# Performance work log

Hardware: AMD Instinct MI355X
Metric: run time of the kernel (lower is better)

## Reference

```python
import jax, jax.numpy as jnp
import numpy as np
import math

B, V, D = 16, 4096, 512
K, H = 64, 8
DK = D // H
DE = 16
DFF = 4 * D
EPS_MASK = 1e-6
EPS_DEN = 1e-8


def setup_inputs() -> dict:
    key = jax.random.key(0)
    ks = jax.random.split(key, 16)
    s = 0.02
    return {
        "x": jax.random.normal(ks[0], (B, V, D), jnp.float32),
        "assign": jax.random.uniform(ks[1], (B, V, K), jnp.float32),
        "E": jax.random.normal(ks[2], (K, DE), jnp.float32),
        "cls0": jax.random.normal(ks[3], (1, K, D), jnp.float32) * s,
        "E2D_w": jax.random.normal(ks[4], (DE, D), jnp.float32) * s,
        "E2D_b": jnp.zeros((D,), jnp.float32),
        "Wq_w": jax.random.normal(ks[5], (D, D), jnp.float32) * s,
        "Wq_b": jnp.zeros((D,), jnp.float32),
        "Wk_w": jax.random.normal(ks[6], (D, D), jnp.float32) * s,
        "Wk_b": jnp.zeros((D,), jnp.float32),
        "Wv_w": jax.random.normal(ks[7], (D, D), jnp.float32) * s,
        "Wv_b": jnp.zeros((D,), jnp.float32),
        "ln_g": jnp.ones((D,), jnp.float32),
        "ln_b": jnp.zeros((D,), jnp.float32),
        "fc1_w": jax.random.normal(ks[8], (D, DFF), jnp.float32) * s,
        "fc1_b": jnp.zeros((DFF,), jnp.float32),
        "fc2_w": jax.random.normal(ks[9], (DFF, D), jnp.float32) * s,
        "fc2_b": jnp.zeros((D,), jnp.float32),
    }


def _layernorm(x, g, b):
    mu = x.mean(-1, keepdims=True)
    var = ((x - mu) ** 2).mean(-1, keepdims=True)
    return (x - mu) / jnp.sqrt(var + 1e-5) * g + b


def reference(x, assign, E, cls0, E2D_w, E2D_b, Wq_w, Wq_b, Wk_w, Wk_b, Wv_w, Wv_b,
              ln_g, ln_b, fc1_w, fc1_b, fc2_w, fc2_b):
    # CLS tokens modulated by module embeddings: [B,K,D]
    cls = jnp.broadcast_to(cls0, (B, K, D)) + (E @ E2D_w + E2D_b)[None]

    # detached mask (transpose of assign): [B,K,V]
    mask_kv = jax.lax.stop_gradient(jnp.swapaxes(assign, 1, 2))
    count_per_k = mask_kv.sum(-1)                 # [B,K]
    empty_mask = count_per_k <= 1e-6              # [B,K]

    # projections -> heads
    q = (_layernorm(cls, ln_g, ln_b) @ Wq_w + Wq_b).reshape(B, K, H, DK)
    k = (x @ Wk_w + Wk_b).reshape(B, V, H, DK)
    v = (x @ Wv_w + Wv_b).reshape(B, V, H, DK)

    # logits [B,H,K,V]
    logits = jnp.einsum("bkhd,bvhd->bhkv", q, k) / math.sqrt(DK)
    log_mask = jnp.log(jnp.clip(mask_kv, 0.0, 1.0) + EPS_MASK)[:, None]  # [B,1,K,V]
    scores = logits + log_mask
    scores = scores - scores.max(-1, keepdims=True)
    attn = jnp.exp(scores)
    attn = attn / (attn.sum(-1, keepdims=True) + EPS_DEN)

    # weighted values, merge heads -> [B,K,D]
    m = jnp.einsum("bhkv,bvhd->bkhd", attn, v).reshape(B, K, D)

    # empty-slot fallback
    m = jnp.where(empty_mask[..., None], cls, m)

    # FFN residual (LayerNorm shared with q path); eval mode: dropout off
    h = _layernorm(m, ln_g, ln_b)
    h = jax.nn.gelu(h @ fc1_w + fc1_b, approximate=False) @ fc2_w + fc2_b
    m = m + h
    return m, count_per_k, empty_mask
```

## Files before the change

kernel.cpp:

```cpp
#include <hip/hip_runtime.h>
#include <hip/hip_bf16.h>
#include <cstdint>
#include <cmath>

#define DEV static __device__ __forceinline__

typedef __attribute__((ext_vector_type(8))) short bf16x8;
typedef __attribute__((ext_vector_type(4))) float f32x4;

DEV ushort f2bf(float f) {
    union { float f; uint32_t u; } v; v.f = f;
    uint32_t r = v.u + 0x7FFFu + ((v.u >> 16) & 1u);
    return (ushort)(r >> 16);
}
DEV uint32_t pack2bf(float lo, float hi) {
    return (uint32_t)f2bf(lo) | ((uint32_t)f2bf(hi) << 16);
}
DEV float bf2f(ushort h) {
    union { uint32_t u; float f; } v; v.u = ((uint32_t)h) << 16;
    return v.f;
}
DEV void gld16(const ushort* g, ushort* l) {
    __builtin_amdgcn_global_load_lds(
        (const __attribute__((address_space(1))) unsigned int*)g,
        (__attribute__((address_space(3))) unsigned int*)l, 16, 0, 0);
}

__global__ __launch_bounds__(256)
void prep_all_k(int nxb, const float* __restrict__ x, ushort* __restrict__ xb,
                const float* __restrict__ E, const float* __restrict__ cls0,
                const float* __restrict__ e2dw, const float* __restrict__ e2db,
                const float* __restrict__ lng, const float* __restrict__ lnbv,
                const float* __restrict__ wq, const float* __restrict__ wqb,
                float* __restrict__ cls, ushort* __restrict__ qbf,
                const float* __restrict__ wk, const float* __restrict__ wv,
                const float* __restrict__ fc1w, const float* __restrict__ fc2w,
                const float* __restrict__ kb, const float* __restrict__ vb,
                ushort* __restrict__ wkvt, ushort* __restrict__ fc1t,
                ushort* __restrict__ fc2t, float* __restrict__ biaskv,
                const float* __restrict__ assign, float* __restrict__ cpart)
{
    __shared__ float sh[64 * 65];
    int id = blockIdx.x;
    const int tid = threadIdx.x;

    if (id < nxb) {
        const size_t i = (size_t)id * 256 + tid;
        const float4* s = (const float4*)(x + i * 8);
        float4 a = s[0], b = s[1];
        uint4 o;
        o.x = pack2bf(a.x, a.y); o.y = pack2bf(a.z, a.w);
        o.z = pack2bf(b.x, b.y); o.w = pack2bf(b.z, b.w);
        *(uint4*)(xb + i * 8) = o;
        return;
    }
    id -= nxb;
    if (id < 64) {
        const int k = id;
        float* lnv = sh;
        float* Ek = sh + 512;
        float2* red = (float2*)(sh + 544);
        if (tid < 16) Ek[tid] = E[k * 16 + tid];
        __syncthreads();
        float vals[2];
#pragma unroll
        for (int j = 0; j < 2; j++) {
            int d = tid + j * 256;
            float a = cls0[k * 512 + d] + e2db[d];
#pragma unroll
            for (int e = 0; e < 16; e++) a += Ek[e] * e2dw[e * 512 + d];
            vals[j] = a;
            cls[k * 512 + d] = a;
        }
        red[tid] = make_float2(vals[0] + vals[1],
                               vals[0] * vals[0] + vals[1] * vals[1]);
        __syncthreads();
        for (int s2 = 128; s2 > 0; s2 >>= 1) {
            if (tid < s2) {
                float2 o = red[tid + s2];
                float2 m = red[tid];
                red[tid] = make_float2(m.x + o.x, m.y + o.y);
            }
            __syncthreads();
        }
        float2 sr = red[0];
        float mu = sr.x * (1.f / 512.f);
        float var = sr.y * (1.f / 512.f) - mu * mu;
        float inv = rsqrtf(var + 1e-5f);
        __syncthreads();
#pragma unroll
        for (int j = 0; j < 2; j++) {
            int d = tid + j * 256;
            lnv[d] = (vals[j] - mu) * inv * lng[d] + lnbv[d];
        }
        __syncthreads();
#pragma unroll
        for (int j = 0; j < 2; j++) {
            int n = tid + j * 256;
            float acc = 0.f;
            for (int d = 0; d < 512; ++d)
                acc += lnv[d] * wq[d * 512 + n];
            qbf[k * 512 + n] = f2bf(acc + wqb[n]);
        }
        return;
    }
    id -= 64;
    if (id < 2564) {
        if (id >= 2560) {
            int i = (id - 2560) * 256 + tid;
            biaskv[i] = (i < 512) ? kb[i] : vb[i - 512];
            return;
        }
        const float* in; ushort* out; int R, C, bx, by;
        if (id < 256)        { in = wk;   out = wkvt;             R = 512;  C = 512;  int t = id;        bx = t & 15; by = t >> 4; }
        else if (id < 512)   { in = wv;   out = wkvt + 512 * 512; R = 512;  C = 512;  int t = id - 256;  bx = t & 15; by = t >> 4; }
        else if (id < 1536)  { in = fc1w; out = fc1t;             R = 512;  C = 2048; int t = id - 512;  bx = t & 63; by = t >> 6; }
        else                 { in = fc2w; out = fc2t;             R = 2048; C = 512;  int t = id - 1536; bx = t & 15; by = t >> 4; }
        float (*T)[33] = (float (*)[33])sh;
        const int c0 = bx * 32, r0 = by * 32;
        const int tx = tid & 31, ty = tid >> 5;
#pragma unroll
        for (int i = 0; i < 32; i += 8)
            T[ty + i][tx] = in[(size_t)(r0 + ty + i) * C + c0 + tx];
        __syncthreads();
#pragma unroll
        for (int i = 0; i < 32; i += 8)
            out[(size_t)(c0 + ty + i) * R + r0 + tx] = f2bf(T[tx][ty + i]);
        return;
    }
    id -= 2564;
    {
        const int vt = id & 63, b = id >> 6;
        float (*T)[65] = (float (*)[65])sh;
        const int rr = tid >> 2, sg = tid & 3;
        const float4* src = (const float4*)(assign + ((size_t)b * 4096 + vt * 64 + rr) * 64 + sg * 16);
        float4 a0 = src[0], a1 = src[1], a2 = src[2], a3 = src[3];
        float* tr = &T[rr][sg * 16];
        tr[0] = a0.x; tr[1] = a0.y; tr[2] = a0.z; tr[3] = a0.w;
        tr[4] = a1.x; tr[5] = a1.y; tr[6] = a1.z; tr[7] = a1.w;
        tr[8] = a2.x; tr[9] = a2.y; tr[10] = a2.z; tr[11] = a2.w;
        tr[12] = a3.x; tr[13] = a3.y; tr[14] = a3.z; tr[15] = a3.w;
        __syncthreads();
        const int k = rr;
        float ssum = 0.f;
#pragma unroll
        for (int j = 0; j < 4; j++)
#pragma unroll
            for (int t2 = 0; t2 < 4; t2++) ssum += T[sg * 16 + j * 4 + t2][k];
        ssum += __shfl_xor(ssum, 1, 64);
        ssum += __shfl_xor(ssum, 2, 64);
        if (sg == 0) cpart[((size_t)b * 64 + k) * 64 + vt] = ssum;
    }
}

template<int AMODE, int EPI, int SWZ, int ND, int KD, int LDK>
__global__ __launch_bounds__(512)
void gemm_k(const void* __restrict__ Ap, const ushort* __restrict__ Bt,
            const float* __restrict__ bias,
            ushort* __restrict__ o_bf, const float* __restrict__ res,
            float* __restrict__ o_f)
{
    __shared__ ushort smem[16384];
    ushort* As = smem;
    ushort* Bs = smem + 8192;
    int m0, n0;
    if (SWZ) {
        int L = blockIdx.x;
        int c = L & 7, j = L >> 3;
        m0 = (c * 64 + (j >> 3)) * 128;
        n0 = (j & 7) * 128;
    } else {
        m0 = blockIdx.x * 128;
        n0 = blockIdx.y * 128;
    }
    const int tid = threadIdx.x;
    const int w = tid >> 6, l = tid & 63;
    const int wr = w >> 2, wc = w & 3;
    const int lg = l >> 4, lr = l & 15;

    const f32x4 fzero = {0.f, 0.f, 0.f, 0.f};
    f32x4 acc[4][2];
#pragma unroll
    for (int i = 0; i < 4; i++)
#pragma unroll
        for (int j = 0; j < 2; j++) acc[i][j] = fzero;

    const int lrow8 = l >> 3;
    const int colswz = ((l & 7) ^ lrow8) * 8;
    const ushort* gB  = Bt + (size_t)(n0 + w * 16 + lrow8) * LDK + colswz;
    const ushort* gA0 = (const ushort*)Ap + (size_t)(m0 + w * 16 + lrow8) * LDK + colswz;
    const float*  gA1 = (const float*)Ap + (size_t)(m0 + w * 16 + (l >> 2)) * LDK + (l & 3) * 16;

    const int kbase = blockIdx.z * KD;
    constexpr int NT = KD / 64;
#pragma unroll
    for (int t = 0; t < NT; ++t) {
        const int kt = kbase + t * 64;
        __syncthreads();
        if (AMODE == 0) {
#pragma unroll
            for (int i = 0; i < 2; i++) {
                gld16(gA0 + (size_t)i * 8 * LDK + kt, As + (w * 16 + i * 8) * 64);
                gld16(gB + (size_t)i * 8 * LDK + kt, Bs + (w * 16 + i * 8) * 64);
            }
        } else {
            float4 av[4];
#pragma unroll
            for (int i = 0; i < 4; i++)
                av[i] = *(const float4*)(gA1 + kt + i * 4);
#pragma unroll
            for (int i = 0; i < 2; i++)
                gld16(gB + (size_t)i * 8 * LDK + kt, Bs + (w * 16 + i * 8) * 64);
            {
                int r = w * 16 + (l >> 2);
                uint2 p0, p1;
                p0.x = pack2bf(av[0].x, av[0].y); p0.y = pack2bf(av[0].z, av[0].w);
                uint2 q0; q0.x = pack2bf(av[1].x, av[1].y); q0.y = pack2bf(av[1].z, av[1].w);
                p1.x = pack2bf(av[2].x, av[2].y); p1.y = pack2bf(av[2].z, av[2].w);
                uint2 q1; q1.x = pack2bf(av[3].x, av[3].y); q1.y = pack2bf(av[3].z, av[3].w);
                int cb = (l & 3) * 32;
                *(uint2*)((char*)As + r * 128 + ((cb     ) ^ ((r & 7) << 4))) = p0;
                *(uint2*)((char*)As + r * 128 + ((cb +  8) ^ ((r & 7) << 4))) = q0;
                *(uint2*)((char*)As + r * 128 + ((cb + 16) ^ ((r & 7) << 4))) = p1;
                *(uint2*)((char*)As + r * 128 + ((cb + 24) ^ ((r & 7) << 4))) = q1;
            }
        }
        asm volatile("s_waitcnt vmcnt(0)" ::: "memory");
        __syncthreads();
#pragma unroll
        for (int kk = 0; kk < 2; kk++) {
            int kb = (kk * 32 + lg * 8) * 2;
            bf16x8 af[4], bfv[2];
#pragma unroll
            for (int mi = 0; mi < 4; mi++) {
                int row = wr * 64 + mi * 16 + lr;
                af[mi] = *(bf16x8*)((char*)As + row * 128 + (kb ^ ((row & 7) << 4)));
            }
#pragma unroll
            for (int ni = 0; ni < 2; ni++) {
                int row = wc * 32 + ni * 16 + lr;
                bfv[ni] = *(bf16x8*)((char*)Bs + row * 128 + (kb ^ ((row & 7) << 4)));
            }
#pragma unroll
            for (int mi = 0; mi < 4; mi++)
#pragma unroll
                for (int ni = 0; ni < 2; ni++)
                    acc[mi][ni] = __builtin_amdgcn_mfma_f32_16x16x32_bf16(af[mi], bfv[ni], acc[mi][ni], 0, 0, 0);
        }
    }

    if (EPI == 0) {
        __syncthreads();
#pragma unroll
        for (int mi = 0; mi < 4; mi++)
#pragma unroll
            for (int ni = 0; ni < 2; ni++)
#pragma unroll
                for (int r = 0; r < 4; r++) {
                    int rl = wr * 64 + mi * 16 + lg * 4 + r;
                    int cl = wc * 32 + ni * 16 + lr;
                    int byteoff = rl * 256 + ((cl * 2) ^ ((rl & 7) << 4));
                    *(ushort*)((char*)smem + byteoff) = f2bf(acc[mi][ni][r] + bias[n0 + cl]);
                }
        __syncthreads();
        const int row = tid >> 2, sg2 = tid & 3;
        uint4* dq = (uint4*)(o_bf + (size_t)(m0 + row) * ND + n0 + sg2 * 32);
#pragma unroll
        for (int q2 = 0; q2 < 4; q2++) {
            int byteoff = row * 256 + ((sg2 * 64 + q2 * 16) ^ ((row & 7) << 4));
            dq[q2] = *(const uint4*)((char*)smem + byteoff);
        }
    } else {
        float* ofz = o_f;
        if (EPI == 3)
            ofz = o_f + (size_t)blockIdx.z * (size_t)gridDim.x * 128 * ND;
#pragma unroll
        for (int mi = 0; mi < 4; mi++) {
#pragma unroll
            for (int ni = 0; ni < 2; ni++) {
#pragma unroll
                for (int r = 0; r < 4; r++) {
                    int row = m0 + wr * 64 + mi * 16 + lg * 4 + r;
                    int col = n0 + wc * 32 + ni * 16 + lr;
                    if (EPI == 1) {
                        float c = acc[mi][ni][r] + bias[col];
                        float gg = 0.5f * c * (1.f + erff(c * 0.70710678f));
                        o_bf[(size_t)row * ND + col] = f2bf(gg);
                    } else if (EPI == 2) {
                        float c = acc[mi][ni][r] + bias[col];
                        o_f[(size_t)row * ND + col] = c + res[(size_t)row * ND + col];
                    } else {
                        ofz[(size_t)row * ND + col] = acc[mi][ni][r];
                    }
                }
            }
        }
    }
}

__global__ __launch_bounds__(256)
void combine2_k(const float* __restrict__ fcp, const float* __restrict__ fc2b,
                float* __restrict__ mout)
{
    const int i = blockIdx.x * 256 + threadIdx.x;
    const int col = i & 511;
    float s = fc2b[col] + fcp[i] + fcp[i + 524288] + fcp[i + 2 * 524288] + fcp[i + 3 * 524288];
    mout[i] += s;
}

__global__ __launch_bounds__(256)
void attn_k(const ushort* __restrict__ qbf, const ushort* __restrict__ kv,
            const float* __restrict__ assign,
            float* __restrict__ partO, float* __restrict__ partML)
{
    const int h = blockIdx.x, s = blockIdx.y, b = blockIdx.z;
    __shared__ ushort Qs[64 * 64];
    __shared__ ushort Ks[64 * 64];
    __shared__ ushort Vt[64 * 64];
    __shared__ ushort Ps[64 * 64];
    __shared__ float  Lm[64 * 64];
    const int tid = threadIdx.x;
    const int w = tid >> 6, l = tid & 63, lg = l >> 4, lr = l & 15;
    const int rr = tid >> 2, qt = tid & 3;

    {
        const uint4* src = (const uint4*)(qbf + rr * 512 + h * 64 + qt * 16);
        uint4 t0 = src[0], t1 = src[1];
        int kb = qt * 32;
        *(uint4*)((char*)Qs + rr * 128 + ( kb       ^ ((rr & 7) << 4))) = t0;
        *(uint4*)((char*)Qs + rr * 128 + ((kb + 16) ^ ((rr & 7) << 4))) = t1;
    }

    const f32x4 fzero = {0.f, 0.f, 0.f, 0.f};
    f32x4 oacc[4];
#pragma unroll
    for (int ni = 0; ni < 4; ni++) oacc[ni] = fzero;
    float m_run[4], l_run[4];
#pragma unroll
    for (int r = 0; r < 4; r++) { m_run[r] = -3e38f; l_run[r] = 0.f; }

    const int v00 = s * 1024;

    for (int c = 0; c < 16; ++c) {
        const int vb = v00 + c * 64;
        __syncthreads();
        {
            const size_t rowb = ((size_t)b * 4096 + vb + rr) * 1024 + h * 64;
            const uint4* srck = (const uint4*)(kv + rowb + qt * 16);
            uint4 k0 = srck[0], k1 = srck[1];
            int kb = qt * 32;
            *(uint4*)((char*)Ks + rr * 128 + ( kb       ^ ((rr & 7) << 4))) = k0;
            *(uint4*)((char*)Ks + rr * 128 + ((kb + 16) ^ ((rr & 7) << 4))) = k1;
            const ushort* srcv = kv + rowb + 512 + qt * 16;
            ushort vvv[16];
            *(uint4*)&vvv[0] = ((const uint4*)srcv)[0];
            *(uint4*)&vvv[8] = ((const uint4*)srcv)[1];
#pragma unroll
            for (int i = 0; i < 16; i++) {
                int dk = qt * 16 + i;
                *(ushort*)((char*)Vt + dk * 128 + ((rr * 2) ^ ((dk & 7) << 4))) = vvv[i];
            }
            const float4* srca = (const float4*)(assign + ((size_t)b * 4096 + vb + rr) * 64 + qt * 16);
            float4 A0 = srca[0], A1 = srca[1], A2 = srca[2], A3 = srca[3];
            float av[16] = {A0.x, A0.y, A0.z, A0.w, A1.x, A1.y, A1.z, A1.w,
                            A2.x, A2.y, A2.z, A2.w, A3.x, A3.y, A3.z, A3.w};
#pragma unroll
            for (int i = 0; i < 16; i++)
                Lm[(qt * 16 + i) * 64 + rr] = __logf(fminf(fmaxf(av[i], 0.f), 1.f) + 1e-6f);
        }
        __syncthreads();

        f32x4 sacc[4];
#pragma unroll
        for (int ni = 0; ni < 4; ni++) sacc[ni] = fzero;
        __builtin_amdgcn_s_setprio(1);
#pragma unroll
        for (int kk = 0; kk < 2; kk++) {
            int kb = (kk * 32 + lg * 8) * 2;
            int qrow = w * 16 + lr;
            bf16x8 aq = *(bf16x8*)((char*)Qs + qrow * 128 + (kb ^ ((qrow & 7) << 4)));
#pragma unroll
            for (int ni = 0; ni < 4; ni++) {
                int kr = ni * 16 + lr;
                bf16x8 bk = *(bf16x8*)((char*)Ks + kr * 128 + (kb ^ ((kr & 7) << 4)));
                sacc[ni] = __builtin_amdgcn_mfma_f32_16x16x32_bf16(aq, bk, sacc[ni], 0, 0, 0);
            }
        }
        __builtin_amdgcn_s_setprio(0);
        float sv[4][4], mx[4];
#pragma unroll
        for (int r = 0; r < 4; r++) {
            int q = w * 16 + lg * 4 + r;
            float m_ = -3e38f;
#pragma unroll
            for (int ni = 0; ni < 4; ni++) {
                float xx = sacc[ni][r] * 0.125f + Lm[q * 64 + ni * 16 + lr];
                sv[ni][r] = xx;
                m_ = fmaxf(m_, xx);
            }
            mx[r] = m_;
        }
#pragma unroll
        for (int off = 1; off < 16; off <<= 1)
#pragma unroll
            for (int r = 0; r < 4; r++) mx[r] = fmaxf(mx[r], __shfl_xor(mx[r], off, 64));
        float scale[4], lad[4];
#pragma unroll
        for (int r = 0; r < 4; r++) {
            float mn = fmaxf(m_run[r], mx[r]);
            scale[r] = __expf(m_run[r] - mn);
            m_run[r] = mn;
            float ls = 0.f;
#pragma unroll
            for (int ni = 0; ni < 4; ni++) {
                float p = __expf(sv[ni][r] - mn);
                sv[ni][r] = p;
                ls += p;
            }
            lad[r] = ls;
        }
#pragma unroll
        for (int off = 1; off < 16; off <<= 1)
#pragma unroll
            for (int r = 0; r < 4; r++) lad[r] += __shfl_xor(lad[r], off, 64);
#pragma unroll
        for (int r = 0; r < 4; r++) l_run[r] = l_run[r] * scale[r] + lad[r];
#pragma unroll
        for (int ni = 0; ni < 4; ni++) {
            f32x4 o = oacc[ni];
            o[0] *= scale[0]; o[1] *= scale[1]; o[2] *= scale[2]; o[3] *= scale[3];
            oacc[ni] = o;
        }
#pragma unroll
        for (int ni = 0; ni < 4; ni++)
#pragma unroll
            for (int r = 0; r < 4; r++) {
                int q = w * 16 + lg * 4 + r;
                int key = ni * 16 + lr;
                *(ushort*)((char*)Ps + q * 128 + ((key * 2) ^ ((q & 7) << 4))) = f2bf(sv[ni][r]);
            }
        __builtin_amdgcn_s_setprio(1);
#pragma unroll
        for (int kk = 0; kk < 2; kk++) {
            int kb = (kk * 32 + lg * 8) * 2;
            int prow = w * 16 + lr;
            bf16x8 ap = *(bf16x8*)((char*)Ps + prow * 128 + (kb ^ ((prow & 7) << 4)));
#pragma unroll
            for (int ni = 0; ni < 4; ni++) {
                int dk = ni * 16 + lr;
                bf16x8 bv = *(bf16x8*)((char*)Vt + dk * 128 + (kb ^ ((dk & 7) << 4)));
                oacc[ni] = __builtin_amdgcn_mfma_f32_16x16x32_bf16(ap, bv, oacc[ni], 0, 0, 0);
            }
        }
        __builtin_amdgcn_s_setprio(0);
    }
    const size_t ob = ((size_t)((b * 8 + h) * 4 + s)) * 4096;
#pragma unroll
    for (int ni = 0; ni < 4; ni++)
#pragma unroll
        for (int r = 0; r < 4; r++) {
            int q = w * 16 + lg * 4 + r;
            int dk = ni * 16 + lr;
            partO[ob + q * 64 + dk] = oacc[ni][r];
        }
    if (lr == 0) {
#pragma unroll
        for (int r = 0; r < 4; r++) {
            int q = w * 16 + lg * 4 + r;
            partML[((b * 8 + h) * 4 + s) * 128 + q * 2 + 0] = m_run[r];
            partML[((b * 8 + h) * 4 + s) * 128 + q * 2 + 1] = l_run[r];
        }
    }
}

__global__ __launch_bounds__(256)
void combine_k(const float* __restrict__ partO, const float* __restrict__ partML,
               const float* __restrict__ cls, const float* __restrict__ cpart,
               float* __restrict__ cnt, float* __restrict__ emp,
               float* __restrict__ mout)
{
    const int bh = blockIdx.x, b = bh >> 3, h = bh & 7;
    __shared__ float Ms[64], Ls[64], Cs[64];
    const int tid = threadIdx.x;
    if (tid < 64) {
        float M = -3e38f;
#pragma unroll
        for (int s2 = 0; s2 < 4; s2++) M = fmaxf(M, partML[(bh * 4 + s2) * 128 + tid * 2]);
        float L = 0.f;
#pragma unroll
        for (int s2 = 0; s2 < 4; s2++) {
            float m_ = partML[(bh * 4 + s2) * 128 + tid * 2];
            float l_ = partML[(bh * 4 + s2) * 128 + tid * 2 + 1];
            L += l_ * __expf(m_ - M);
        }
        Ms[tid] = M; Ls[tid] = L;
        const float4* p = (const float4*)(cpart + ((size_t)b * 64 + tid) * 64);
        float cs = 0.f;
#pragma unroll
        for (int t = 0; t < 16; t++) {
            float4 f = p[t];
            cs += f.x + f.y + f.z + f.w;
        }
        Cs[tid] = cs;
        if (h == 0) {
            cnt[b * 64 + tid] = cs;
            emp[b * 64 + tid] = (cs <= 1e-6f) ? 1.f : 0.f;
        }
    }
    __syncthreads();
#pragma unroll
    for (int i = 0; i < 16; i++) {
        int e = i * 256 + tid;
        int q = e >> 6, dk = e & 63;
        float o = 0.f;
#pragma unroll
        for (int s2 = 0; s2 < 4; s2++) {
            float m_ = partML[(bh * 4 + s2) * 128 + q * 2];
            o += partO[(size_t)(bh * 4 + s2) * 4096 + e] * __expf(m_ - Ms[q]);
        }
        float val = o / (Ls[q] + 1e-8f);
        if (Cs[q] <= 1e-6f) val = cls[q * 512 + h * 64 + dk];
        mout[((size_t)b * 64 + q) * 512 + h * 64 + dk] = val;
    }
}

__global__ __launch_bounds__(256)
void ln_rows_k(const float* __restrict__ m, const float* __restrict__ g,
               const float* __restrict__ be, ushort* __restrict__ out)
{
    const int r = blockIdx.x, tid = threadIdx.x;
    float v0 = m[(size_t)r * 512 + tid];
    float v1 = m[(size_t)r * 512 + tid + 256];
    __shared__ float2 red[256];
    red[tid] = make_float2(v0 + v1, v0 * v0 + v1 * v1);
    __syncthreads();
    for (int s2 = 128; s2 > 0; s2 >>= 1) {
        if (tid < s2) {
            float2 o = red[tid + s2];
            float2 m2 = red[tid];
            red[tid] = make_float2(m2.x + o.x, m2.y + o.y);
        }
        __syncthreads();
    }
    float2 sr = red[0];
    float mu = sr.x * (1.f / 512.f);
    float var = sr.y * (1.f / 512.f) - mu * mu;
    float inv = rsqrtf(var + 1e-5f);
    out[(size_t)r * 512 + tid]       = f2bf((v0 - mu) * inv * g[tid] + be[tid]);
    out[(size_t)r * 512 + tid + 256] = f2bf((v1 - mu) * inv * g[tid + 256] + be[tid + 256]);
}

extern "C" void kernel_launch(void* const* d_in, const int* in_sizes, int n_in,
                              void* d_out, int out_size, void* d_ws, size_t ws_size,
                              hipStream_t stream)
{
    const float* x      = (const float*)d_in[0];
    const float* assign = (const float*)d_in[1];
    const float* E      = (const float*)d_in[2];
    const float* cls0   = (const float*)d_in[3];
    const float* e2dw   = (const float*)d_in[4];
    const float* e2db   = (const float*)d_in[5];
    const float* wq     = (const float*)d_in[6];
    const float* wqb    = (const float*)d_in[7];
    const float* wk     = (const float*)d_in[8];
    const float* wkb    = (const float*)d_in[9];
    const float* wv     = (const float*)d_in[10];
    const float* wvb    = (const float*)d_in[11];
    const float* lng    = (const float*)d_in[12];
    const float* lnbv   = (const float*)d_in[13];
    const float* fc1w   = (const float*)d_in[14];
    const float* fc1b   = (const float*)d_in[15];
    const float* fc2w   = (const float*)d_in[16];
    const float* fc2b   = (const float*)d_in[17];

    float* mout = (float*)d_out;
    float* cnt  = mout + (size_t)16 * 64 * 512;
    float* emp  = cnt + 16 * 64;

    char* ws = (char*)d_ws;
    size_t off = 0;
    auto alloc = [&](size_t bytes) -> char* {
        char* p = ws + off;
        off = (off + bytes + 255) & ~(size_t)255;
        return p;
    };
    float*  cls    = (float*) alloc((size_t)64 * 512 * 4);
    ushort* qbf    = (ushort*)alloc((size_t)64 * 512 * 2);
    ushort* wkvt   = (ushort*)alloc((size_t)1024 * 512 * 2);
    float*  biaskv = (float*) alloc((size_t)1024 * 4);
    ushort* fc1t   = (ushort*)alloc((size_t)2048 * 512 * 2);
    ushort* fc2t   = (ushort*)alloc((size_t)512 * 2048 * 2);
    ushort* kvb    = (ushort*)alloc((size_t)16 * 4096 * 1024 * 2);
    float*  partO  = (float*) alloc((size_t)16 * 8 * 4 * 64 * 64 * 4);
    float*  partML = (float*) alloc((size_t)16 * 8 * 4 * 128 * 4);
    float*  cpart  = (float*) alloc((size_t)16 * 64 * 64 * 4);
    ushort* lnbf   = (ushort*)alloc((size_t)1024 * 512 * 2);
    ushort* hhb    = (ushort*)alloc((size_t)1024 * 2048 * 2);
    float*  fcp    = (float*) alloc((size_t)4 * 1024 * 512 * 4);
    ushort* xb     = (ushort*)alloc((size_t)16 * 4096 * 512 * 2);
    const bool use_xb = (off <= ws_size);

    const int nxb = use_xb ? 16384 : 0;
    prep_all_k<<<nxb + 64 + 2564 + 1024, 256, 0, stream>>>(
        nxb, x, xb, E, cls0, e2dw, e2db, lng, lnbv, wq, wqb, cls, qbf,
        wk, wv, fc1w, fc2w, wkb, wvb, wkvt, fc1t, fc2t, biaskv,
        assign, cpart);

    if (use_xb) {
        gemm_k<0, 0, 1, 1024, 512, 512><<<4096, 512, 0, stream>>>(xb, wkvt, biaskv,
                                                                  kvb, nullptr, nullptr);
    } else {
        gemm_k<1, 0, 1, 1024, 512, 512><<<4096, 512, 0, stream>>>(x, wkvt, biaskv,
                                                                  kvb, nullptr, nullptr);
    }
    attn_k<<<dim3(8, 4, 16), 256, 0, stream>>>(qbf, kvb, assign, partO, partML);
    combine_k<<<128, 256, 0, stream>>>(partO, partML, cls, cpart, cnt, emp, mout);
    ln_rows_k<<<1024, 256, 0, stream>>>(mout, lng, lnbv, lnbf);
    gemm_k<0, 1, 0, 2048, 512, 512><<<dim3(8, 16), 512, 0, stream>>>(lnbf, fc1t, fc1b,
                                                                     hhb, nullptr, nullptr);
    gemm_k<0, 3, 0, 512, 512, 2048><<<dim3(8, 4, 4), 512, 0, stream>>>(hhb, fc2t, fc2b,
                                                                       nullptr, nullptr, fcp);
    combine2_k<<<2048, 256, 0, stream>>>(fcp, fc2b, mout);
}
```

Baseline: 275.0 us.

## Fuse fp32-to-bf16 x conversion into KV GEMM via direct-to-LDS fp32 loads

Removes the separate pass that converted x to a bf16 buffer in the prep kernel. The KV projection GEMM now loads fp32 x tiles straight into LDS with global_load_lds using an XOR swizzle, then converts to bf16 with packed cvt instructions when building MFMA fragments. This drops a full write and re-read of the 64 MB bf16 copy of x. In exchange the GEMM reads twice as many A bytes per tile, needs more LDS per block, and does conversion work that is repeated for each of the 8 N-tiles.

```diff
diff --git a/kernel.cpp b/kernel.cpp
--- a/kernel.cpp
+++ b/kernel.cpp
@@ -13,9 +13,6 @@
     uint32_t r = v.u + 0x7FFFu + ((v.u >> 16) & 1u);
     return (ushort)(r >> 16);
 }
-DEV uint32_t pack2bf(float lo, float hi) {
-    return (uint32_t)f2bf(lo) | ((uint32_t)f2bf(hi) << 16);
-}
 DEV float bf2f(ushort h) {
     union { uint32_t u; float f; } v; v.u = ((uint32_t)h) << 16;
     return v.f;
@@ -25,10 +22,19 @@
         (const __attribute__((address_space(1))) unsigned int*)g,
         (__attribute__((address_space(3))) unsigned int*)l, 16, 0, 0);
 }
+DEV bf16x8 cvt8(float4 a, float4 b) {
+    uint32_t u0, u1, u2, u3;
+    asm("v_cvt_pk_bf16_f32 %0, %1, %2" : "=v"(u0) : "v"(a.x), "v"(a.y));
+    asm("v_cvt_pk_bf16_f32 %0, %1, %2" : "=v"(u1) : "v"(a.z), "v"(a.w));
+    asm("v_cvt_pk_bf16_f32 %0, %1, %2" : "=v"(u2) : "v"(b.x), "v"(b.y));
+    asm("v_cvt_pk_bf16_f32 %0, %1, %2" : "=v"(u3) : "v"(b.z), "v"(b.w));
+    union { uint4 u; bf16x8 h; } r;
+    r.u = make_uint4(u0, u1, u2, u3);
+    return r.h;
+}
 
 __global__ __launch_bounds__(256)
-void prep_all_k(int nxb, const float* __restrict__ x, ushort* __restrict__ xb,
-                const float* __restrict__ E, const float* __restrict__ cls0,
+void prep_all_k(const float* __restrict__ E, const float* __restrict__ cls0,
                 const float* __restrict__ e2dw, const float* __restrict__ e2db,
                 const float* __restrict__ lng, const float* __restrict__ lnbv,
                 const float* __restrict__ wq, const float* __restrict__ wqb,
@@ -44,17 +50,6 @@
     int id = blockIdx.x;
     const int tid = threadIdx.x;
 
-    if (id < nxb) {
-        const size_t i = (size_t)id * 256 + tid;
-        const float4* s = (const float4*)(x + i * 8);
-        float4 a = s[0], b = s[1];
-        uint4 o;
-        o.x = pack2bf(a.x, a.y); o.y = pack2bf(a.z, a.w);
-        o.z = pack2bf(b.x, b.y); o.w = pack2bf(b.z, b.w);
-        *(uint4*)(xb + i * 8) = o;
-        return;
-    }
-    id -= nxb;
     if (id < 64) {
         const int k = id;
         float* lnv = sh;
@@ -160,9 +155,10 @@
             ushort* __restrict__ o_bf, const float* __restrict__ res,
             float* __restrict__ o_f)
 {
-    __shared__ ushort smem[16384];
-    ushort* As = smem;
-    ushort* Bs = smem + 8192;
+    __shared__ ushort smem[(AMODE == 2) ? 24576 : 16384];
+    float*  Asf = (float*)smem;
+    ushort* As  = smem;
+    ushort* Bs  = smem + ((AMODE == 2) ? 16384 : 8192);
     int m0, n0;
     if (SWZ) {
         int L = blockIdx.x;
@@ -189,7 +185,13 @@
     const int colswz = ((l & 7) ^ lrow8) * 8;
     const ushort* gB  = Bt + (size_t)(n0 + w * 16 + lrow8) * LDK + colswz;
     const ushort* gA0 = (const ushort*)Ap + (size_t)(m0 + w * 16 + lrow8) * LDK + colswz;
-    const float*  gA1 = (const float*)Ap + (size_t)(m0 + w * 16 + (l >> 2)) * LDK + (l & 3) * 16;
+    const float* gA2[4];
+#pragma unroll
+    for (int i = 0; i < 4; i++) {
+        int rloc = i * 4 + (l >> 4);
+        gA2[i] = (const float*)Ap + (size_t)(m0 + w * 16 + rloc) * LDK
+                 + (((l & 15) ^ rloc) << 2);
+    }
 
     const int kbase = blockIdx.z * KD;
     constexpr int NT = KD / 64;
@@ -204,42 +206,43 @@
                 gld16(gB + (size_t)i * 8 * LDK + kt, Bs + (w * 16 + i * 8) * 64);
             }
         } else {
-            float4 av[4];
 #pragma unroll
             for (int i = 0; i < 4; i++)
-                av[i] = *(const float4*)(gA1 + kt + i * 4);
+                gld16((const ushort*)(gA2[i] + kt), (ushort*)(Asf + (w * 16 + i * 4) * 64));
 #pragma unroll
             for (int i = 0; i < 2; i++)
                 gld16(gB + (size_t)i * 8 * LDK + kt, Bs + (w * 16 + i * 8) * 64);
+        }
+        asm volatile("s_waitcnt vmcnt(0)" ::: "memory");
+        __syncthreads();
+#pragma unroll
+        for (int kk = 0; kk < 2; kk++) {
+            bf16x8 af[4], bfv[2];
+            if (AMODE == 2) {
+                const int c0 = kk * 8 + lg * 2;
+#pragma unroll
+                for (int mi = 0; mi < 4; mi++) {
+                    int row = wr * 64 + mi * 16 + lr;
+                    const float* base = Asf + row * 64;
+                    float4 fa = *(const float4*)(base + ((c0 ^ lr) << 2));
+                    float4 fb = *(const float4*)(base + (((c0 + 1) ^ lr) << 2));
+                    af[mi] = cvt8(fa, fb);
+                }
+            } else {
+                int kb = (kk * 32 + lg * 8) * 2;
+#pragma unroll
+                for (int mi = 0; mi < 4; mi++) {
+                    int row = wr * 64 + mi * 16 + lr;
+                    af[mi] = *(bf16x8*)((char*)As + row * 128 + (kb ^ ((row & 7) << 4)));
+                }
+            }
             {
-                int r = w * 16 + (l >> 2);
-                uint2 p0, p1;
-                p0.x = pack2bf(av[0].x, av[0].y); p0.y = pack2bf(av[0].z, av[0].w);
-                uint2 q0; q0.x = pack2bf(av[1].x, av[1].y); q0.y = pack2bf(av[1].z, av[1].w);
-                p1.x = pack2bf(av[2].x, av[2].y); p1.y = pack2bf(av[2].z, av[2].w);
-                uint2 q1; q1.x = pack2bf(av[3].x, av[3].y); q1.y = pack2bf(av[3].z, av[3].w);
-                int cb = (l & 3) * 32;
-                *(uint2*)((char*)As + r * 128 + ((cb     ) ^ ((r & 7) << 4))) = p0;
-                *(uint2*)((char*)As + r * 128 + ((cb +  8) ^ ((r & 7) << 4))) = q0;
-                *(uint2*)((char*)As + r * 128 + ((cb + 16) ^ ((r & 7) << 4))) = p1;
-                *(uint2*)((char*)As + r * 128 + ((cb + 24) ^ ((r & 7) << 4))) = q1;
-            }
-        }
-        asm volatile("s_waitcnt vmcnt(0)" ::: "memory");
-        __syncthreads();
-#pragma unroll
-        for (int kk = 0; kk < 2; kk++) {
-            int kb = (kk * 32 + lg * 8) * 2;
-            bf16x8 af[4], bfv[2];
-#pragma unroll
-            for (int mi = 0; mi < 4; mi++) {
-                int row = wr * 64 + mi * 16 + lr;
-                af[mi] = *(bf16x8*)((char*)As + row * 128 + (kb ^ ((row & 7) << 4)));
-            }
-#pragma unroll
-            for (int ni = 0; ni < 2; ni++) {
-                int row = wc * 32 + ni * 16 + lr;
-                bfv[ni] = *(bf16x8*)((char*)Bs + row * 128 + (kb ^ ((row & 7) << 4)));
+                int kb = (kk * 32 + lg * 8) * 2;
+#pragma unroll
+                for (int ni = 0; ni < 2; ni++) {
+                    int row = wc * 32 + ni * 16 + lr;
+                    bfv[ni] = *(bf16x8*)((char*)Bs + row * 128 + (kb ^ ((row & 7) << 4)));
+                }
             }
 #pragma unroll
             for (int mi = 0; mi < 4; mi++)
@@ -597,22 +600,15 @@
     ushort* lnbf   = (ushort*)alloc((size_t)1024 * 512 * 2);
     ushort* hhb    = (ushort*)alloc((size_t)1024 * 2048 * 2);
     float*  fcp    = (float*) alloc((size_t)4 * 1024 * 512 * 4);
-    ushort* xb     = (ushort*)alloc((size_t)16 * 4096 * 512 * 2);
-    const bool use_xb = (off <= ws_size);
-
-    const int nxb = use_xb ? 16384 : 0;
-    prep_all_k<<<nxb + 64 + 2564 + 1024, 256, 0, stream>>>(
-        nxb, x, xb, E, cls0, e2dw, e2db, lng, lnbv, wq, wqb, cls, qbf,
+    (void)ws_size;
+
+    prep_all_k<<<64 + 2564 + 1024, 256, 0, stream>>>(
+        E, cls0, e2dw, e2db, lng, lnbv, wq, wqb, cls, qbf,
         wk, wv, fc1w, fc2w, wkb, wvb, wkvt, fc1t, fc2t, biaskv,
         assign, cpart);
 
-    if (use_xb) {
-        gemm_k<0, 0, 1, 1024, 512, 512><<<4096, 512, 0, stream>>>(xb, wkvt, biaskv,
-                                                                  kvb, nullptr, nullptr);
-    } else {
-        gemm_k<1, 0, 1, 1024, 512, 512><<<4096, 512, 0, stream>>>(x, wkvt, biaskv,
-                                                                  kvb, nullptr, nullptr);
-    }
+    gemm_k<2, 0, 1, 1024, 512, 512><<<4096, 512, 0, stream>>>(x, wkvt, biaskv,
+                                                              kvb, nullptr, nullptr);
     attn_k<<<dim3(8, 4, 16), 256, 0, stream>>>(qbf, kvb, assign, partO, partML);
     combine_k<<<128, 256, 0, stream>>>(partO, partML, cls, cpart, cnt, emp, mout);
     ln_rows_k<<<1024, 256, 0, stream>>>(mout, lng, lnbv, lnbf);
```

Measured after the change: 312.0 us. +13.4%, slower.
